# Kernel tuning notes

Hardware: AMD Instinct MI355X
Metric: run time of the kernel (lower is better)

The kernel has to match this reference:

```python
import jax, jax.numpy as jnp
import numpy as np

LEN_PARTS = 6
FRAME_MASK_RATIO = 0.4
JOINT_MASK_RATIO = 0.5
LEAKY_SLOPE = 0.1


def leaky_relu(x):
    return jnp.where(x >= 0, x, LEAKY_SLOPE * x)


def setup_inputs() -> dict:
    key = jax.random.key(0)
    ks = jax.random.split(key, 8)
    N, C, T, V, M = 256, 2, 120, 13, 1
    len_keep = int(T * (1.0 - FRAME_MASK_RATIO))  # 72
    return {
        "x": jax.random.normal(ks[0], (N, C, T, V, M), jnp.float32),
        "frame_noise": jax.random.uniform(ks[1], (N * M, T), jnp.float32),
        "joint_noise": jax.random.uniform(ks[2], (N * M, len_keep, V), jnp.float32),
        "pos_embed": jax.random.normal(ks[3], (1, C, T, V), jnp.float32) * 0.02,
        "dec_pos_embed": jax.random.normal(ks[4], (1, 256, T, V), jnp.float32) * 0.02,
        "w_in": jax.random.normal(ks[5], (64, C), jnp.float32) * (1.0 / np.sqrt(C)),
        "b_in": jnp.zeros((64,), jnp.float32),
        "w_enc": jax.random.normal(ks[6], (256, 64), jnp.float32) * (1.0 / np.sqrt(64)),
        "w_dec": jax.random.normal(ks[7], (2, 256), jnp.float32) * (1.0 / np.sqrt(256)),
    }


def reference(x, frame_noise, joint_noise, pos_embed, dec_pos_embed, w_in, b_in, w_enc, w_dec):
    N, C, T, V, M = x.shape  # M == 1 (required by final view in the original code)
    NM = N * M
    # [N,C,T,V,M] -> [N*M,C,T,V]
    x2 = jnp.transpose(x, (0, 4, 1, 2, 3)).reshape(NM, C, T, V)
    xp = x2 + pos_embed

    # ---- mask_frames: per-sample random frame subset (argsort + gather) ----
    len_keep = int(T * (1.0 - FRAME_MASK_RATIO))  # 72
    ids_shuffle = jnp.argsort(frame_noise, axis=1)            # [NM,T]
    ids_keep = jnp.sort(ids_shuffle[:, :len_keep], axis=1)    # [NM,72]
    ids_mask = jnp.sort(ids_shuffle[:, len_keep:], axis=1)    # [NM,48]
    frame_ids = jnp.concatenate([ids_keep, ids_mask], axis=1)  # [NM,T]
    xm = jnp.take_along_axis(xp, ids_keep[:, None, :, None], axis=2)  # [NM,C,72,V]

    # ---- mask_joints: per-(sample,frame) random joint subset, fully vectorized ----
    n_mask = int(V * JOINT_MASK_RATIO)  # 6
    n_keep = V - n_mask                  # 7
    jperm = jnp.argsort(joint_noise, axis=-1)         # [NM,72,V] random perm per (n,t)
    mask_idx = jperm[..., :n_mask]                     # [NM,72,6]
    # boolean joint mask [NM,72,V]
    jmask = jnp.any(mask_idx[..., None] == jnp.arange(V), axis=-2)
    # stable argsort of bool: kept (False) indices ascending, then masked ascending
    combined = jnp.argsort(jmask, axis=-1, stable=True)  # [NM,72,V] == joint_ids_restore
    keep_ids = combined[..., :n_keep]                     # [NM,72,7]
    x_masked = jnp.take_along_axis(xm, keep_ids[:, None, :, :], axis=3)  # [NM,C,72,7]

    # ---- fold parts and embed: [NM,C,72,7] -> [NM,C,12,42] ----
    Tm, Vm = len_keep, n_keep
    xf = x_masked.reshape(NM, C, Tm // LEN_PARTS, Vm * LEN_PARTS)
    h = jnp.einsum('oc,nctv->notv', w_in, xf) + b_in[None, :, None, None]
    h = leaky_relu(h)
    # encoder (STA blocks replaced by channel projection; source unavailable)
    e = leaky_relu(jnp.einsum('oc,nctv->notv', w_enc, h))  # [NM,256,12,42]

    # ---- reconstruct_data: scatter masked tokens back via fancy gathers ----
    Ne, Ce, Te, Ve = e.shape
    e2 = e.reshape(Ne, Ce, Te * LEN_PARTS, Ve // LEN_PARTS)   # [NM,256,72,7]
    e2 = jnp.transpose(e2, (0, 2, 3, 1))                       # [NM,72,7,256]
    e2 = jnp.concatenate([e2, jnp.zeros((Ne, Tm, n_mask, Ce), e2.dtype)], axis=2)  # [NM,72,13,256]
    r = jnp.take_along_axis(e2, combined[..., None], axis=2)   # [NM,72,13,256]
    r = jnp.concatenate([r, jnp.zeros((Ne, T - Tm, V, Ce), r.dtype)], axis=1)      # [NM,120,13,256]
    r = jnp.take_along_axis(r, frame_ids[:, :, None, None], axis=1)                # [NM,120,13,256]
    r = jnp.transpose(r, (0, 3, 1, 2))                          # [NM,256,120,13]

    decoded = r + dec_pos_embed
    d = decoded.reshape(N, Ce, T // LEN_PARTS, V * LEN_PARTS)  # [N,256,20,78]
    # decoder (STA blocks replaced by channel projection to out_channels=2)
    out = jnp.einsum('oc,nctv->notv', w_dec, d)                 # [N,2,20,78]
    return out.reshape(N, C, T, V, M)
```

## Files before the change

### kernel.cpp

```cpp
#include <hip/hip_runtime.h>
#include <hip/hip_bf16.h>

#define N_SAMP 256
#define C_IN 2
#define T_FRAMES 120
#define V_JOINTS 13
#define LEN_KEEP 72
#define N_MASK_J 6
#define N_KEEP_J 7
#define H_DIM 64
#define E_DIM 256
#define POS_PER_SAMPLE (T_FRAMES * V_JOINTS)
#define NPOS (LEN_KEEP * N_KEEP_J)
#define NROW 512
#define NPT (NROW / 16)
#define THREADS 512

typedef __attribute__((ext_vector_type(8))) __bf16 bf16x8;
typedef __attribute__((ext_vector_type(4))) float f32x4;

__global__ __launch_bounds__(256)
void prep_kernel(const float* __restrict__ w_dec,
                 const float* __restrict__ dec_pos_embed,
                 const float* __restrict__ w_enc,
                 float* __restrict__ dpeproj,
                 __bf16* __restrict__ wbf)
{
    int bid = blockIdx.x;
    int tid = threadIdx.x;
    if (bid < 13) {
        int i = bid * 256 + tid;
        if (i < C_IN * POS_PER_SAMPLE) {
            int o = i / POS_PER_SAMPLE;
            int p = i - o * POS_PER_SAMPLE;
            float s = 0.f;
            for (int c = 0; c < E_DIM; ++c)
                s += w_dec[o * E_DIM + c] * dec_pos_embed[c * POS_PER_SAMPLE + p];
            dpeproj[i] = s;
        }
    } else {
        int i = (bid - 13) * 256 + tid;
        if (i < E_DIM * H_DIM) wbf[i] = (__bf16)w_enc[i];
    }
}

__global__ __launch_bounds__(THREADS, 1)
void fused_kernel(const float* __restrict__ x,
                  const float* __restrict__ pos_embed,
                  const float* __restrict__ w_in,
                  const float* __restrict__ b_in,
                  const __bf16* __restrict__ wbf,
                  const float* __restrict__ w_dec,
                  const float* __restrict__ dpeproj,
                  const float* __restrict__ frame_noise,
                  const float* __restrict__ joint_noise,
                  float* __restrict__ out)
{
    __shared__ __align__(16) char h_raw[NROW * 128];
    __shared__ float2 xm_sh[NROW];
    __shared__ int src_sh[NPOS];
    __shared__ short rev_sh[POS_PER_SAMPLE];
    __shared__ float pdpart[4][NPOS][2];
    __shared__ float noise_sh[T_FRAMES];
    __shared__ int rank_sh[T_FRAMES];
    __shared__ int ids_keep_sh[LEN_KEEP];
    __shared__ int tout_sh[LEN_KEEP];

    int n = blockIdx.x;
    int tid = threadIdx.x;
    int lane = tid & 63, wave = tid >> 6;
    int g = lane >> 4;
    int r16 = lane & 15;
    int ctg = wave & 3;
    int ptg = wave >> 2;

    bf16x8 wfr[4][2];
    f32x4 wd0r[4], wd1r[4];
    {
        const bf16x8* wq = (const bf16x8*)wbf;
        #pragma unroll
        for (int i = 0; i < 4; ++i) {
            int ct = ctg * 4 + i;
            wfr[i][0] = wq[(ct * 16 + r16) * 8 + 0 + g];
            wfr[i][1] = wq[(ct * 16 + r16) * 8 + 4 + g];
            wd0r[i] = *(const f32x4*)(w_dec + ct * 16 + g * 4);
            wd1r[i] = *(const f32x4*)(w_dec + E_DIM + ct * 16 + g * 4);
        }
    }

    if (tid < T_FRAMES) noise_sh[tid] = frame_noise[n * T_FRAMES + tid];
    for (int i = tid; i < POS_PER_SAMPLE; i += THREADS) rev_sh[i] = -1;
    __syncthreads();

    if (tid < T_FRAMES) {
        float v = noise_sh[tid];
        int r = 0;
        for (int j = 0; j < T_FRAMES; ++j) {
            float u = noise_sh[j];
            r += (u < v || (u == v && j < tid)) ? 1 : 0;
        }
        rank_sh[tid] = r;
    }
    __syncthreads();

    if (tid < T_FRAMES) {
        int kc = 0;
        for (int j = 0; j < tid; ++j) kc += (rank_sh[j] < LEN_KEEP) ? 1 : 0;
        if (rank_sh[tid] < LEN_KEEP) ids_keep_sh[kc] = tid;
        if (tid < LEN_KEEP)
            tout_sh[tid] = (rank_sh[tid] < LEN_KEEP) ? kc : LEN_KEEP + (tid - kc);
    }
    __syncthreads();

    if (tid < LEN_KEEP) {
        int f = tid;
        const float* jn = joint_noise + (n * LEN_KEEP + f) * V_JOINTS;
        float jv[V_JOINTS];
        for (int v = 0; v < V_JOINTS; ++v) jv[v] = jn[v];
        int jrank[V_JOINTS];
        for (int v = 0; v < V_JOINTS; ++v) {
            int r = 0;
            for (int u = 0; u < V_JOINTS; ++u)
                r += (jv[u] < jv[v] || (jv[u] == jv[v] && u < v)) ? 1 : 0;
            jrank[v] = r;
        }
        int comb[V_JOINTS];
        int idx = 0;
        for (int v = 0; v < V_JOINTS; ++v) if (jrank[v] >= N_MASK_J) comb[idx++] = v;
        for (int v = 0; v < V_JOINTS; ++v) if (jrank[v] <  N_MASK_J) comb[idx++] = v;
        int vout[N_KEEP_J];
        for (int v = 0; v < V_JOINTS; ++v) {
            int s = comb[v];
            if (s < N_KEEP_J) vout[s] = v;
        }
        int tsrc = ids_keep_sh[f];
        int tout = tout_sh[f];
        for (int s = 0; s < N_KEEP_J; ++s) {
            int p = f * N_KEEP_J + s;
            src_sh[p] = tsrc * V_JOINTS + comb[s];
            int d = tout * V_JOINTS + vout[s];
            rev_sh[d] = (short)p;
        }
    }
    __syncthreads();

    if (tid < NROW) {
        if (tid < NPOS) {
            int so = src_sh[tid];
            float x0 = x[(n * 2 + 0) * POS_PER_SAMPLE + so] + pos_embed[so];
            float x1 = x[(n * 2 + 1) * POS_PER_SAMPLE + so] + pos_embed[POS_PER_SAMPLE + so];
            xm_sh[tid] = make_float2(x0, x1);
        } else {
            xm_sh[tid] = make_float2(0.f, 0.f);
        }
    }
    __syncthreads();

    {
        int kq = lane;
        float wi0 = w_in[kq * 2 + 0], wi1 = w_in[kq * 2 + 1], bk = b_in[kq];
        for (int p = wave; p < NROW; p += 8) {
            float2 xm = xm_sh[p];
            float hv = fmaf(wi0, xm.x, fmaf(wi1, xm.y, bk));
            hv = fmaxf(hv, 0.1f * hv);
            int off = (p * 128 + kq * 2) ^ ((p & 7) << 4);
            *(__bf16*)(h_raw + off) = (__bf16)hv;
        }
    }
    __syncthreads();

    for (int t = 0; t < 16; ++t) {
        int pt = ptg * 16 + t;
        int row = pt * 16 + r16;
        int swz = (row & 7) << 4;
        bf16x8 b0 = *(const bf16x8*)(h_raw + ((row * 128 + g * 16) ^ swz));
        bf16x8 b1 = *(const bf16x8*)(h_raw + ((row * 128 + 64 + g * 16) ^ swz));

        float pd0 = 0.f, pd1 = 0.f;
        #pragma unroll
        for (int i = 0; i < 4; ++i) {
            f32x4 acc = {0.f, 0.f, 0.f, 0.f};
            acc = __builtin_amdgcn_mfma_f32_16x16x32_bf16(wfr[i][0], b0, acc, 0, 0, 0);
            acc = __builtin_amdgcn_mfma_f32_16x16x32_bf16(wfr[i][1], b1, acc, 0, 0, 0);
            #pragma unroll
            for (int r = 0; r < 4; ++r) {
                float e = acc[r];
                e = fmaxf(e, 0.1f * e);
                pd0 = fmaf(wd0r[i][r], e, pd0);
                pd1 = fmaf(wd1r[i][r], e, pd1);
            }
        }
        pd0 += __shfl_xor(pd0, 16); pd0 += __shfl_xor(pd0, 32);
        pd1 += __shfl_xor(pd1, 16); pd1 += __shfl_xor(pd1, 32);

        int p = pt * 16 + r16;
        if (lane < 16 && p < NPOS) {
            pdpart[ctg][p][0] = pd0;
            pdpart[ctg][p][1] = pd1;
        }
    }
    __syncthreads();

    {
        float* outn = out + n * C_IN * POS_PER_SAMPLE;
        for (int i = tid; i < C_IN * POS_PER_SAMPLE; i += THREADS) {
            int o = (i >= POS_PER_SAMPLE) ? 1 : 0;
            int pos = i - o * POS_PER_SAMPLE;
            float v = dpeproj[i];
            int p = rev_sh[pos];
            if (p >= 0)
                v += pdpart[0][p][o] + pdpart[1][p][o]
                   + pdpart[2][p][o] + pdpart[3][p][o];
            outn[i] = v;
        }
    }
}

extern "C" void kernel_launch(void* const* d_in, const int* in_sizes, int n_in,
                              void* d_out, int out_size, void* d_ws, size_t ws_size,
                              hipStream_t stream) {
    const float* x             = (const float*)d_in[0];
    const float* frame_noise   = (const float*)d_in[1];
    const float* joint_noise   = (const float*)d_in[2];
    const float* pos_embed     = (const float*)d_in[3];
    const float* dec_pos_embed = (const float*)d_in[4];
    const float* w_in          = (const float*)d_in[5];
    const float* b_in          = (const float*)d_in[6];
    const float* w_enc         = (const float*)d_in[7];
    const float* w_dec         = (const float*)d_in[8];
    float* out = (float*)d_out;

    float* dpeproj = (float*)d_ws;
    __bf16* wbf    = (__bf16*)(dpeproj + C_IN * POS_PER_SAMPLE);

    prep_kernel<<<77, 256, 0, stream>>>(w_dec, dec_pos_embed, w_enc, dpeproj, wbf);

    fused_kernel<<<N_SAMP, THREADS, 0, stream>>>(
        x, pos_embed, w_in, b_in, wbf, w_dec, dpeproj,
        frame_noise, joint_noise, out);
}
```

Before: 37.01 us.

## Move per-sample mask index computation into prep kernel blocks

The frame ranking and joint permutation logic, which runs serially at the start of each fused block, moves into 256 extra blocks of the prep kernel. These blocks run alongside the dpeproj and weight-conversion blocks and write source indices and reverse maps to workspace, which the fused kernel then loads from global memory. This shortens the serial prologue of the main kernel, at the cost of an extra global round trip for the index tables and a larger prep grid. Small unroll pragmas are also added to the prep loops.

```diff
diff --git a/kernel.cpp b/kernel.cpp
--- a/kernel.cpp
+++ b/kernel.cpp
@@ -23,25 +23,101 @@
 void prep_kernel(const float* __restrict__ w_dec,
                  const float* __restrict__ dec_pos_embed,
                  const float* __restrict__ w_enc,
+                 const float* __restrict__ frame_noise,
+                 const float* __restrict__ joint_noise,
                  float* __restrict__ dpeproj,
-                 __bf16* __restrict__ wbf)
+                 __bf16* __restrict__ wbf,
+                 int* __restrict__ srcg,
+                 short* __restrict__ revg)
 {
     int bid = blockIdx.x;
     int tid = threadIdx.x;
+
     if (bid < 13) {
         int i = bid * 256 + tid;
         if (i < C_IN * POS_PER_SAMPLE) {
             int o = i / POS_PER_SAMPLE;
             int p = i - o * POS_PER_SAMPLE;
             float s = 0.f;
+            #pragma unroll 4
             for (int c = 0; c < E_DIM; ++c)
                 s += w_dec[o * E_DIM + c] * dec_pos_embed[c * POS_PER_SAMPLE + p];
             dpeproj[i] = s;
         }
-    } else {
+        return;
+    }
+    if (bid < 77) {
         int i = (bid - 13) * 256 + tid;
         if (i < E_DIM * H_DIM) wbf[i] = (__bf16)w_enc[i];
-    }
+        return;
+    }
+
+    int n = bid - 77;
+    __shared__ float noise_sh[T_FRAMES];
+    __shared__ int rank_sh[T_FRAMES];
+    __shared__ int ids_keep_sh[LEN_KEEP];
+    __shared__ int tout_sh[LEN_KEEP];
+    __shared__ short rev_sh[POS_PER_SAMPLE];
+
+    if (tid < T_FRAMES) noise_sh[tid] = frame_noise[n * T_FRAMES + tid];
+    for (int i = tid; i < POS_PER_SAMPLE; i += 256) rev_sh[i] = -1;
+    __syncthreads();
+
+    if (tid < T_FRAMES) {
+        float v = noise_sh[tid];
+        int r = 0;
+        #pragma unroll 4
+        for (int j = 0; j < T_FRAMES; ++j) {
+            float u = noise_sh[j];
+            r += (u < v || (u == v && j < tid)) ? 1 : 0;
+        }
+        rank_sh[tid] = r;
+    }
+    __syncthreads();
+
+    if (tid < T_FRAMES) {
+        int kc = 0;
+        #pragma unroll 4
+        for (int j = 0; j < tid; ++j) kc += (rank_sh[j] < LEN_KEEP) ? 1 : 0;
+        if (rank_sh[tid] < LEN_KEEP) ids_keep_sh[kc] = tid;
+        if (tid < LEN_KEEP)
+            tout_sh[tid] = (rank_sh[tid] < LEN_KEEP) ? kc : LEN_KEEP + (tid - kc);
+    }
+    __syncthreads();
+
+    if (tid < LEN_KEEP) {
+        int f = tid;
+        const float* jn = joint_noise + (n * LEN_KEEP + f) * V_JOINTS;
+        float jv[V_JOINTS];
+        for (int v = 0; v < V_JOINTS; ++v) jv[v] = jn[v];
+        int jrank[V_JOINTS];
+        for (int v = 0; v < V_JOINTS; ++v) {
+            int r = 0;
+            for (int u = 0; u < V_JOINTS; ++u)
+                r += (jv[u] < jv[v] || (jv[u] == jv[v] && u < v)) ? 1 : 0;
+            jrank[v] = r;
+        }
+        int comb[V_JOINTS];
+        int idx = 0;
+        for (int v = 0; v < V_JOINTS; ++v) if (jrank[v] >= N_MASK_J) comb[idx++] = v;
+        for (int v = 0; v < V_JOINTS; ++v) if (jrank[v] <  N_MASK_J) comb[idx++] = v;
+        int vout[N_KEEP_J];
+        for (int v = 0; v < V_JOINTS; ++v) {
+            int s = comb[v];
+            if (s < N_KEEP_J) vout[s] = v;
+        }
+        int tsrc = ids_keep_sh[f];
+        int tout = tout_sh[f];
+        for (int s = 0; s < N_KEEP_J; ++s) {
+            int p = f * N_KEEP_J + s;
+            srcg[n * NPOS + p] = tsrc * V_JOINTS + comb[s];
+            rev_sh[tout * V_JOINTS + vout[s]] = (short)p;
+        }
+    }
+    __syncthreads();
+
+    for (int i = tid; i < POS_PER_SAMPLE; i += 256)
+        revg[n * POS_PER_SAMPLE + i] = rev_sh[i];
 }
 
 __global__ __launch_bounds__(THREADS, 1)
@@ -52,19 +128,14 @@
                   const __bf16* __restrict__ wbf,
                   const float* __restrict__ w_dec,
                   const float* __restrict__ dpeproj,
-                  const float* __restrict__ frame_noise,
-                  const float* __restrict__ joint_noise,
+                  const int* __restrict__ srcg,
+                  const short* __restrict__ revg,
                   float* __restrict__ out)
 {
     __shared__ __align__(16) char h_raw[NROW * 128];
     __shared__ float2 xm_sh[NROW];
-    __shared__ int src_sh[NPOS];
     __shared__ short rev_sh[POS_PER_SAMPLE];
     __shared__ float pdpart[4][NPOS][2];
-    __shared__ float noise_sh[T_FRAMES];
-    __shared__ int rank_sh[T_FRAMES];
-    __shared__ int ids_keep_sh[LEN_KEEP];
-    __shared__ int tout_sh[LEN_KEEP];
 
     int n = blockIdx.x;
     int tid = threadIdx.x;
@@ -88,65 +159,9 @@
         }
     }
 
-    if (tid < T_FRAMES) noise_sh[tid] = frame_noise[n * T_FRAMES + tid];
-    for (int i = tid; i < POS_PER_SAMPLE; i += THREADS) rev_sh[i] = -1;
-    __syncthreads();
-
-    if (tid < T_FRAMES) {
-        float v = noise_sh[tid];
-        int r = 0;
-        for (int j = 0; j < T_FRAMES; ++j) {
-            float u = noise_sh[j];
-            r += (u < v || (u == v && j < tid)) ? 1 : 0;
-        }
-        rank_sh[tid] = r;
-    }
-    __syncthreads();
-
-    if (tid < T_FRAMES) {
-        int kc = 0;
-        for (int j = 0; j < tid; ++j) kc += (rank_sh[j] < LEN_KEEP) ? 1 : 0;
-        if (rank_sh[tid] < LEN_KEEP) ids_keep_sh[kc] = tid;
-        if (tid < LEN_KEEP)
-            tout_sh[tid] = (rank_sh[tid] < LEN_KEEP) ? kc : LEN_KEEP + (tid - kc);
-    }
-    __syncthreads();
-
-    if (tid < LEN_KEEP) {
-        int f = tid;
-        const float* jn = joint_noise + (n * LEN_KEEP + f) * V_JOINTS;
-        float jv[V_JOINTS];
-        for (int v = 0; v < V_JOINTS; ++v) jv[v] = jn[v];
-        int jrank[V_JOINTS];
-        for (int v = 0; v < V_JOINTS; ++v) {
-            int r = 0;
-            for (int u = 0; u < V_JOINTS; ++u)
-                r += (jv[u] < jv[v] || (jv[u] == jv[v] && u < v)) ? 1 : 0;
-            jrank[v] = r;
-        }
-        int comb[V_JOINTS];
-        int idx = 0;
-        for (int v = 0; v < V_JOINTS; ++v) if (jrank[v] >= N_MASK_J) comb[idx++] = v;
-        for (int v = 0; v < V_JOINTS; ++v) if (jrank[v] <  N_MASK_J) comb[idx++] = v;
-        int vout[N_KEEP_J];
-        for (int v = 0; v < V_JOINTS; ++v) {
-            int s = comb[v];
-            if (s < N_KEEP_J) vout[s] = v;
-        }
-        int tsrc = ids_keep_sh[f];
-        int tout = tout_sh[f];
-        for (int s = 0; s < N_KEEP_J; ++s) {
-            int p = f * N_KEEP_J + s;
-            src_sh[p] = tsrc * V_JOINTS + comb[s];
-            int d = tout * V_JOINTS + vout[s];
-            rev_sh[d] = (short)p;
-        }
-    }
-    __syncthreads();
-
     if (tid < NROW) {
         if (tid < NPOS) {
-            int so = src_sh[tid];
+            int so = srcg[n * NPOS + tid];
             float x0 = x[(n * 2 + 0) * POS_PER_SAMPLE + so] + pos_embed[so];
             float x1 = x[(n * 2 + 1) * POS_PER_SAMPLE + so] + pos_embed[POS_PER_SAMPLE + so];
             xm_sh[tid] = make_float2(x0, x1);
@@ -154,6 +169,8 @@
             xm_sh[tid] = make_float2(0.f, 0.f);
         }
     }
+    for (int i = tid; i < POS_PER_SAMPLE; i += THREADS)
+        rev_sh[i] = revg[n * POS_PER_SAMPLE + i];
     __syncthreads();
 
     {
@@ -232,10 +249,14 @@
 
     float* dpeproj = (float*)d_ws;
     __bf16* wbf    = (__bf16*)(dpeproj + C_IN * POS_PER_SAMPLE);
-
-    prep_kernel<<<77, 256, 0, stream>>>(w_dec, dec_pos_embed, w_enc, dpeproj, wbf);
+    int*   srcg    = (int*)(wbf + E_DIM * H_DIM);
+    short* revg    = (short*)(srcg + N_SAMP * NPOS);
+
+    prep_kernel<<<333, 256, 0, stream>>>(w_dec, dec_pos_embed, w_enc,
+                                         frame_noise, joint_noise,
+                                         dpeproj, wbf, srcg, revg);
 
     fused_kernel<<<N_SAMP, THREADS, 0, stream>>>(
         x, pos_embed, w_in, b_in, wbf, w_dec, dpeproj,
-        frame_noise, joint_noise, out);
+        srcg, revg, out);
 }
```

After: 39.20 us. 5.9% more time.
